# Kernel optimization log

Measured on AMD Instinct MI355X. Metric: run time of the kernel, lower is better.

Reference implementation:

```python
import jax, jax.numpy as jnp
import numpy as np

STEPS = 50   # MattingSolver(steps=50)
H, W = 1024, 1024
EPS = 1e-2   # diagonal regularization (matting lambda-like), guarantees SPD


def _build_laplacian():
    """5-point weighted graph Laplacian + EPS*I on an HxW grid, COO, row-sorted."""
    rng = np.random.RandomState(0)
    n = H * W
    idx = np.arange(n, dtype=np.int32).reshape(H, W)
    wh = rng.rand(H, W - 1).astype(np.float32) + 0.1  # horizontal edge weights
    wv = rng.rand(H - 1, W).astype(np.float32) + 0.1  # vertical edge weights
    a_h, b_h = idx[:, :-1].ravel(), idx[:, 1:].ravel()
    a_v, b_v = idx[:-1, :].ravel(), idx[1:, :].ravel()
    diag_idx = np.arange(n, dtype=np.int32)
    rows = np.concatenate([a_h, b_h, a_v, b_v, diag_idx])
    cols = np.concatenate([b_h, a_h, b_v, a_v, diag_idx])
    off = np.concatenate([wh.ravel(), wh.ravel(), wv.ravel(), wv.ravel()])
    deg = np.zeros(n, dtype=np.float32)
    np.add.at(deg, a_h, wh.ravel()); np.add.at(deg, b_h, wh.ravel())
    np.add.at(deg, a_v, wv.ravel()); np.add.at(deg, b_v, wv.ravel())
    vals = np.concatenate([-off, deg + EPS]).astype(np.float32)
    order = np.argsort(rows, kind='stable')
    return rows[order], cols[order], vals[order]


def setup_inputs() -> dict:
    key = jax.random.key(0)
    rows, cols, vals = _build_laplacian()
    b = jax.random.normal(key, (H * W,), dtype=jnp.float32)
    return {"rows": jnp.asarray(rows), "cols": jnp.asarray(cols),
            "vals": jnp.asarray(vals), "b": b}


def reference(rows, cols, vals, b):
    """Unpreconditioned conjugate gradient: solve A x = b, x0 = 0, STEPS iters."""
    n = b.shape[0]

    def spmv(p):  # y = A @ p via COO gather + segment-sum scatter
        return jax.ops.segment_sum(vals * p[cols], rows, num_segments=n,
                                   indices_are_sorted=True)

    x0 = jnp.zeros_like(b)
    r0 = b                      # r = b - A @ 0
    rs0 = jnp.dot(r0, r0)

    def body(carry, _):
        x, r, p, rs = carry
        Ap = spmv(p)
        alpha = rs / jnp.dot(p, Ap)
        x = x + alpha * p
        r = r - alpha * Ap
        rs_new = jnp.dot(r, r)
        p = r + (rs_new / rs) * p
        return (x, r, p, rs_new), None

    (x, _, _, _), _ = jax.lax.scan(body, (x0, r0, r0, rs0), None, length=STEPS)
    return x
```

## Files before the change

kernel.cpp:

```cpp
#include <hip/hip_runtime.h>

#define HH 1024
#define WW 1024
#define CG_STEPS 50
#define NB 256
#define NT 1024

#define SCOPE __HIP_MEMORY_SCOPE_AGENT
#define POISON64 0xAAAAAAAAAAAAAAAAULL

__device__ __forceinline__ float aload(const float* p) {
    return __hip_atomic_load(p, __ATOMIC_RELAXED, SCOPE);
}
__device__ __forceinline__ void astore(float* p, float v) {
    __hip_atomic_store(p, v, __ATOMIC_RELAXED, SCOPE);
}
__device__ __forceinline__ int iload(const int* p) {
    return __hip_atomic_load(p, __ATOMIC_RELAXED, SCOPE);
}
__device__ __forceinline__ void istore(int* p, int v) {
    __hip_atomic_store(p, v, __ATOMIC_RELAXED, SCOPE);
}
__device__ __forceinline__ unsigned long long uload(const unsigned long long* p) {
    return __hip_atomic_load(p, __ATOMIC_RELAXED, SCOPE);
}
__device__ __forceinline__ void ustore(unsigned long long* p, unsigned long long v) {
    __hip_atomic_store(p, v, __ATOMIC_RELAXED, SCOPE);
}

__device__ __forceinline__ void reduce2T0(float& a, float& b) {
    #pragma unroll
    for (int off = 32; off > 0; off >>= 1) {
        a += __shfl_down(a, off, 64);
        b += __shfl_down(b, off, 64);
    }
    __shared__ float sa[16], sb[16];
    const int lane = threadIdx.x & 63, wid = threadIdx.x >> 6;
    if (lane == 0) { sa[wid] = a; sb[wid] = b; }
    __syncthreads();
    if (threadIdx.x == 0) {
        float ta = 0.f, tb = 0.f;
        #pragma unroll
        for (int i = 0; i < 16; ++i) { ta += sa[i]; tb += sb[i]; }
        a = ta; b = tb;
    }
    __syncthreads();
}

__device__ __forceinline__ void consumeRed(const unsigned long long* red, int k,
                                           float& o1, float& o2) {
    float a = 0.f, b = 0.f;
    if (threadIdx.x < NB) {
        const unsigned long long* q = red + (size_t)k * NB + threadIdx.x;
        unsigned long long v;
        while ((v = uload(q)) == POISON64) __builtin_amdgcn_s_sleep(1);
        a = __uint_as_float((unsigned)(v & 0xFFFFFFFFu));
        b = __uint_as_float((unsigned)(v >> 32));
    }
    #pragma unroll
    for (int off = 32; off > 0; off >>= 1) {
        a += __shfl_down(a, off, 64);
        b += __shfl_down(b, off, 64);
    }
    __shared__ float sa2[16], sb2[16];
    __shared__ float t1, t2;
    const int lane = threadIdx.x & 63, wid = threadIdx.x >> 6;
    if (lane == 0) { sa2[wid] = a; sb2[wid] = b; }
    __syncthreads();
    if (threadIdx.x == 0) {
        float ta = 0.f, tb = 0.f;
        #pragma unroll
        for (int i = 0; i < 16; ++i) { ta += sa2[i]; tb += sb2[i]; }
        t1 = ta; t2 = tb;
    }
    __syncthreads();
    o1 = t1; o2 = t2;
}

__global__ __launch_bounds__(NT)
void cgsolve_kernel(const int* __restrict__ cols, const float* __restrict__ vals,
                    const float* __restrict__ b, float* __restrict__ xout,
                    float* __restrict__ rbuf, unsigned long long* __restrict__ red,
                    int* __restrict__ flags) {
    const int col = threadIdx.x;
    const int bb  = blockIdx.x;

    __shared__ float sr[4][WW + 1];
    __shared__ int   scols[5 * WW];
    __shared__ float svals[5 * WW];

    float adiag[4], art[4], alf[4], adn[4], awu[4];
    float x_[4], r_[4], w_[4], q_[4];
    float p_[4] = {0.f, 0.f, 0.f, 0.f};
    float s_[4] = {0.f, 0.f, 0.f, 0.f};
    float z_[4] = {0.f, 0.f, 0.f, 0.f};

    for (int rr = 0; rr < 4; ++rr) {
        const int i    = 4 * bb + rr;
        const int off  = (i == 0) ? 0 : (4 * WW - 2) + (i - 1) * (5 * WW - 2);
        const int base = 1 + (i > 0) + (i < HH - 1);
        const int len  = base * WW + 2 * WW - 2;
        __syncthreads();
        for (int e = threadIdx.x; e < len; e += NT) {
            scols[e] = cols[off + e];
            svals[e] = vals[off + e];
        }
        __syncthreads();
        const int j      = col;
        const int within = (j == 0) ? 0 : (base + 1) + (j - 1) * (base + 2);
        const int nnz    = base + (j > 0) + (j < WW - 1);
        const int t      = i * WW + j;
        float dg = 0.f, wr = 0.f, wl = 0.f, wd = 0.f, wu = 0.f;
        #pragma unroll
        for (int e = 0; e < 5; ++e) {
            if (e < nnz) {
                const int   c = scols[within + e];
                const float v = svals[within + e];
                if (c == t)           dg = v;
                else if (c == t + 1)  wr = v;
                else if (c == t - 1)  wl = v;
                else if (c == t + WW) wd = v;
                else if (c == t - WW) wu = v;
            }
        }
        adiag[rr] = dg; art[rr] = wr; alf[rr] = wl; adn[rr] = wd; awu[rr] = wu;
        r_[rr] = b[t];
        x_[rr] = 0.f;
    }

    auto applyA = [&](const float* v, float* out, float vtop, float vbot) {
        #pragma unroll
        for (int rr = 0; rr < 4; ++rr) sr[rr][col] = v[rr];
        __syncthreads();
        #pragma unroll
        for (int rr = 0; rr < 4; ++rr) {
            float sum = adiag[rr] * v[rr];
            const float vr = (col < WW - 1) ? sr[rr][col + 1] : 0.f;
            const float vl = (col > 0)      ? sr[rr][col - 1] : 0.f;
            sum += art[rr] * vr + alf[rr] * vl;
            const float vd = (rr < 3) ? v[rr + 1] : vbot;
            const float vu = (rr > 0) ? v[rr - 1] : vtop;
            sum += adn[rr] * vd + awu[rr] * vu;
            out[rr] = sum;
        }
        __syncthreads();
    };

    auto postRed = [&](int k, float rs_l, float dl_l, int flagval) {
        reduce2T0(rs_l, dl_l);
        if (threadIdx.x == 0) {
            istore(&flags[bb], flagval);
            const unsigned long long v =
                ((unsigned long long)__float_as_uint(dl_l) << 32) |
                (unsigned long long)__float_as_uint(rs_l);
            ustore(&red[(size_t)k * NB + bb], v);
        }
    };

    {
        const float btop = (bb > 0)      ? b[(4 * bb - 1) * WW + col] : 0.f;
        const float bbot = (bb < NB - 1) ? b[(4 * bb + 4) * WW + col] : 0.f;
        applyA(r_, w_, btop, bbot);
        astore(&rbuf[(2 * bb + 0) * WW + col], w_[0]);
        astore(&rbuf[(2 * bb + 1) * WW + col], w_[3]);
        float rs_l = 0.f, dl_l = 0.f;
        #pragma unroll
        for (int rr = 0; rr < 4; ++rr) {
            rs_l += r_[rr] * r_[rr];
            dl_l += w_[rr] * r_[rr];
        }
        postRed(0, rs_l, dl_l, 1);
    }

    float gamma_prev = 1.f, alpha_prev = 1.f;

    #pragma unroll 1
    for (int k = 0; k < CG_STEPS; ++k) {
        if (k < CG_STEPS - 1) {
            if (threadIdx.x == 0 && bb > 0)
                while (iload(&flags[bb - 1]) < k + 1) __builtin_amdgcn_s_sleep(1);
            if (threadIdx.x == 1 && bb < NB - 1)
                while (iload(&flags[bb + 1]) < k + 1) __builtin_amdgcn_s_sleep(1);
            __syncthreads();
            const float* hb = rbuf + (size_t)(k & 1) * 2 * NB * WW;
            const float wtop = (bb > 0)
                ? aload(&hb[(2 * (bb - 1) + 1) * WW + col]) : 0.f;
            const float wbot = (bb < NB - 1)
                ? aload(&hb[(2 * (bb + 1) + 0) * WW + col]) : 0.f;
            applyA(w_, q_, wtop, wbot);
        }
        float gam, del;
        consumeRed(red, k, gam, del);

        const float beta  = (k == 0) ? 0.f : gam / gamma_prev;
        const float alpha = (k == 0) ? gam / del
                                     : gam / (del - beta * gam / alpha_prev);
        #pragma unroll
        for (int rr = 0; rr < 4; ++rr) {
            p_[rr] = r_[rr] + beta * p_[rr];
            x_[rr] += alpha * p_[rr];
        }
        if (k == CG_STEPS - 1) break;

        float rs_l = 0.f, dl_l = 0.f;
        #pragma unroll
        for (int rr = 0; rr < 4; ++rr) {
            z_[rr] = q_[rr] + beta * z_[rr];
            s_[rr] = w_[rr] + beta * s_[rr];
            r_[rr] -= alpha * s_[rr];
            w_[rr] -= alpha * z_[rr];
            rs_l += r_[rr] * r_[rr];
            dl_l += w_[rr] * r_[rr];
        }
        float* hbn = rbuf + (size_t)((k + 1) & 1) * 2 * NB * WW;
        astore(&hbn[(2 * bb + 0) * WW + col], w_[0]);
        astore(&hbn[(2 * bb + 1) * WW + col], w_[3]);
        postRed(k + 1, rs_l, dl_l, k + 2);

        gamma_prev = gam; alpha_prev = alpha;
    }

    #pragma unroll
    for (int rr = 0; rr < 4; ++rr)
        xout[(4 * bb + rr) * WW + col] = x_[rr];
}

extern "C" void kernel_launch(void* const* d_in, const int* in_sizes, int n_in,
                              void* d_out, int out_size, void* d_ws, size_t ws_size,
                              hipStream_t stream) {
    const int*   cols = (const int*)d_in[1];
    const float* vals = (const float*)d_in[2];
    const float* b    = (const float*)d_in[3];
    float* x = (float*)d_out;

    float* w    = (float*)d_ws;
    float* rbuf = w;
    unsigned long long* red =
        (unsigned long long*)(rbuf + 2 * 2 * (size_t)NB * WW);
    int* flags = (int*)(red + (size_t)CG_STEPS * NB);


    void* args[] = {(void*)&cols, (void*)&vals, (void*)&b, (void*)&x,
                    (void*)&rbuf, (void*)&red, (void*)&flags};
    hipLaunchCooperativeKernel((void*)cgsolve_kernel, dim3(NB), dim3(NT),
                               args, 0, stream);
}
```

Measured before the change: 307.9 us.

## Drop block barriers by reducing global dot products per wavefront and fusing stencil staging

Each wavefront now polls and sums all 256 per-block partials itself with xor shuffles. This replaces the earlier path where one group of threads loaded, reduced through shared memory and broadcast with two block barriers. The stencil apply is inlined: the shared-memory staging write moves before the neighbour-flag wait, so one barrier serves both, and the trailing barrier is removed. The block partial reduction finishes with a 16-lane shuffle instead of a serial loop by thread 0. The cost is that every wavefront issues its own global polling loads on the reduction buffer, and correctness now depends on later barriers protecting shared-buffer reuse.

```diff
diff --git a/kernel.cpp b/kernel.cpp
--- a/kernel.cpp
+++ b/kernel.cpp
@@ -28,53 +28,32 @@
     __hip_atomic_store(p, v, __ATOMIC_RELAXED, SCOPE);
 }
 
-__device__ __forceinline__ void reduce2T0(float& a, float& b) {
-    #pragma unroll
-    for (int off = 32; off > 0; off >>= 1) {
-        a += __shfl_down(a, off, 64);
-        b += __shfl_down(b, off, 64);
-    }
-    __shared__ float sa[16], sb[16];
-    const int lane = threadIdx.x & 63, wid = threadIdx.x >> 6;
-    if (lane == 0) { sa[wid] = a; sb[wid] = b; }
-    __syncthreads();
-    if (threadIdx.x == 0) {
-        float ta = 0.f, tb = 0.f;
-        #pragma unroll
-        for (int i = 0; i < 16; ++i) { ta += sa[i]; tb += sb[i]; }
-        a = ta; b = tb;
-    }
-    __syncthreads();
-}
-
-__device__ __forceinline__ void consumeRed(const unsigned long long* red, int k,
-                                           float& o1, float& o2) {
+__device__ __forceinline__ void consumeRedWave(const unsigned long long* red,
+                                               int k, float& o1, float& o2) {
+    const int lane = threadIdx.x & 63;
+    const unsigned long long* basep = red + (size_t)k * NB;
+    unsigned long long v[4];
+    #pragma unroll
+    for (int m = 0; m < 4; ++m) v[m] = uload(basep + m * 64 + lane);
+    while (v[0] == POISON64 || v[1] == POISON64 ||
+           v[2] == POISON64 || v[3] == POISON64) {
+        __builtin_amdgcn_s_sleep(1);
+        #pragma unroll
+        for (int m = 0; m < 4; ++m)
+            if (v[m] == POISON64) v[m] = uload(basep + m * 64 + lane);
+    }
     float a = 0.f, b = 0.f;
-    if (threadIdx.x < NB) {
-        const unsigned long long* q = red + (size_t)k * NB + threadIdx.x;
-        unsigned long long v;
-        while ((v = uload(q)) == POISON64) __builtin_amdgcn_s_sleep(1);
-        a = __uint_as_float((unsigned)(v & 0xFFFFFFFFu));
-        b = __uint_as_float((unsigned)(v >> 32));
-    }
-    #pragma unroll
-    for (int off = 32; off > 0; off >>= 1) {
-        a += __shfl_down(a, off, 64);
-        b += __shfl_down(b, off, 64);
-    }
-    __shared__ float sa2[16], sb2[16];
-    __shared__ float t1, t2;
-    const int lane = threadIdx.x & 63, wid = threadIdx.x >> 6;
-    if (lane == 0) { sa2[wid] = a; sb2[wid] = b; }
-    __syncthreads();
-    if (threadIdx.x == 0) {
-        float ta = 0.f, tb = 0.f;
-        #pragma unroll
-        for (int i = 0; i < 16; ++i) { ta += sa2[i]; tb += sb2[i]; }
-        t1 = ta; t2 = tb;
-    }
-    __syncthreads();
-    o1 = t1; o2 = t2;
+    #pragma unroll
+    for (int m = 0; m < 4; ++m) {
+        a += __uint_as_float((unsigned)(v[m] & 0xFFFFFFFFu));
+        b += __uint_as_float((unsigned)(v[m] >> 32));
+    }
+    #pragma unroll
+    for (int mask = 1; mask < 64; mask <<= 1) {
+        a += __shfl_xor(a, mask, 64);
+        b += __shfl_xor(b, mask, 64);
+    }
+    o1 = a; o2 = b;
 }
 
 __global__ __launch_bounds__(NT)
@@ -86,6 +65,7 @@
     const int bb  = blockIdx.x;
 
     __shared__ float sr[4][WW + 1];
+    __shared__ float sa[16], sb[16];
     __shared__ int   scols[5 * WW];
     __shared__ float svals[5 * WW];
 
@@ -128,48 +108,55 @@
         x_[rr] = 0.f;
     }
 
-    auto applyA = [&](const float* v, float* out, float vtop, float vbot) {
-        #pragma unroll
-        for (int rr = 0; rr < 4; ++rr) sr[rr][col] = v[rr];
-        __syncthreads();
+    auto blockPartialPost = [&](int k, float a, float bfl, int flagval) {
+        #pragma unroll
+        for (int mask = 1; mask < 64; mask <<= 1) {
+            a   += __shfl_xor(a,   mask, 64);
+            bfl += __shfl_xor(bfl, mask, 64);
+        }
+        const int lane = threadIdx.x & 63, wid = threadIdx.x >> 6;
+        if (lane == 0) { sa[wid] = a; sb[wid] = bfl; }
+        __syncthreads();
+        if (threadIdx.x < 16) {
+            float ta = sa[threadIdx.x], tb = sb[threadIdx.x];
+            #pragma unroll
+            for (int mask = 1; mask < 16; mask <<= 1) {
+                ta += __shfl_xor(ta, mask, 16);
+                tb += __shfl_xor(tb, mask, 16);
+            }
+            if (threadIdx.x == 0) {
+                const unsigned long long v =
+                    ((unsigned long long)__float_as_uint(tb) << 32) |
+                    (unsigned long long)__float_as_uint(ta);
+                ustore(&red[(size_t)k * NB + bb], v);
+                istore(&flags[bb], flagval);
+            }
+        }
+    };
+
+    {
+        #pragma unroll
+        for (int rr = 0; rr < 4; ++rr) sr[rr][col] = r_[rr];
+        __syncthreads();
+        const float btop = (bb > 0)      ? b[(4 * bb - 1) * WW + col] : 0.f;
+        const float bbot = (bb < NB - 1) ? b[(4 * bb + 4) * WW + col] : 0.f;
+        float rs_l = 0.f, dl_l = 0.f;
         #pragma unroll
         for (int rr = 0; rr < 4; ++rr) {
-            float sum = adiag[rr] * v[rr];
+            float sum = adiag[rr] * r_[rr];
             const float vr = (col < WW - 1) ? sr[rr][col + 1] : 0.f;
             const float vl = (col > 0)      ? sr[rr][col - 1] : 0.f;
             sum += art[rr] * vr + alf[rr] * vl;
-            const float vd = (rr < 3) ? v[rr + 1] : vbot;
-            const float vu = (rr > 0) ? v[rr - 1] : vtop;
+            const float vd = (rr < 3) ? r_[rr + 1] : bbot;
+            const float vu = (rr > 0) ? r_[rr - 1] : btop;
             sum += adn[rr] * vd + awu[rr] * vu;
-            out[rr] = sum;
-        }
-        __syncthreads();
-    };
-
-    auto postRed = [&](int k, float rs_l, float dl_l, int flagval) {
-        reduce2T0(rs_l, dl_l);
-        if (threadIdx.x == 0) {
-            istore(&flags[bb], flagval);
-            const unsigned long long v =
-                ((unsigned long long)__float_as_uint(dl_l) << 32) |
-                (unsigned long long)__float_as_uint(rs_l);
-            ustore(&red[(size_t)k * NB + bb], v);
-        }
-    };
-
-    {
-        const float btop = (bb > 0)      ? b[(4 * bb - 1) * WW + col] : 0.f;
-        const float bbot = (bb < NB - 1) ? b[(4 * bb + 4) * WW + col] : 0.f;
-        applyA(r_, w_, btop, bbot);
+            w_[rr] = sum;
+            rs_l += r_[rr] * r_[rr];
+            dl_l += sum * r_[rr];
+        }
         astore(&rbuf[(2 * bb + 0) * WW + col], w_[0]);
         astore(&rbuf[(2 * bb + 1) * WW + col], w_[3]);
-        float rs_l = 0.f, dl_l = 0.f;
-        #pragma unroll
-        for (int rr = 0; rr < 4; ++rr) {
-            rs_l += r_[rr] * r_[rr];
-            dl_l += w_[rr] * r_[rr];
-        }
-        postRed(0, rs_l, dl_l, 1);
+        blockPartialPost(0, rs_l, dl_l, 1);
     }
 
     float gamma_prev = 1.f, alpha_prev = 1.f;
@@ -177,6 +164,8 @@
     #pragma unroll 1
     for (int k = 0; k < CG_STEPS; ++k) {
         if (k < CG_STEPS - 1) {
+            #pragma unroll
+            for (int rr = 0; rr < 4; ++rr) sr[rr][col] = w_[rr];
             if (threadIdx.x == 0 && bb > 0)
                 while (iload(&flags[bb - 1]) < k + 1) __builtin_amdgcn_s_sleep(1);
             if (threadIdx.x == 1 && bb < NB - 1)
@@ -187,10 +176,21 @@
                 ? aload(&hb[(2 * (bb - 1) + 1) * WW + col]) : 0.f;
             const float wbot = (bb < NB - 1)
                 ? aload(&hb[(2 * (bb + 1) + 0) * WW + col]) : 0.f;
-            applyA(w_, q_, wtop, wbot);
-        }
+            #pragma unroll
+            for (int rr = 0; rr < 4; ++rr) {
+                float sum = adiag[rr] * w_[rr];
+                const float vr = (col < WW - 1) ? sr[rr][col + 1] : 0.f;
+                const float vl = (col > 0)      ? sr[rr][col - 1] : 0.f;
+                sum += art[rr] * vr + alf[rr] * vl;
+                const float vd = (rr < 3) ? w_[rr + 1] : wbot;
+                const float vu = (rr > 0) ? w_[rr - 1] : wtop;
+                sum += adn[rr] * vd + awu[rr] * vu;
+                q_[rr] = sum;
+            }
+        }
+
         float gam, del;
-        consumeRed(red, k, gam, del);
+        consumeRedWave(red, k, gam, del);
 
         const float beta  = (k == 0) ? 0.f : gam / gamma_prev;
         const float alpha = (k == 0) ? gam / del
@@ -215,7 +215,7 @@
         float* hbn = rbuf + (size_t)((k + 1) & 1) * 2 * NB * WW;
         astore(&hbn[(2 * bb + 0) * WW + col], w_[0]);
         astore(&hbn[(2 * bb + 1) * WW + col], w_[3]);
-        postRed(k + 1, rs_l, dl_l, k + 2);
+        blockPartialPost(k + 1, rs_l, dl_l, k + 2);
 
         gamma_prev = gam; alpha_prev = alpha;
     }
```

Measured after the change: 309.8 us. About the same (+0.6%).
